# Kernel optimization log

Measured on AMD Instinct MI355X. Metric: run time of the kernel, lower is better.

The kernel has to match this reference:

```python
import jax, jax.numpy as jnp
import numpy as np

N = 50000   # nodes
E = 800000  # edges
IN, HID, OUT, H = 128, 256, 128, 4
C1 = HID // H  # per-head channels for conv1/conv2
EPS_LN = 1e-5


def layer_norm(x, g, b):
    mu = x.mean(-1, keepdims=True)
    var = ((x - mu) ** 2).mean(-1, keepdims=True)
    return (x - mu) * jax.lax.rsqrt(var + EPS_LN) * g + b


def gatv2(x, src, dst, edge_attr, Wl, bl, Wr, br, We, att, bias, heads, ch, n):
    # PyG GATv2Conv (concat=True, negative_slope=0.2, share_weights=False)
    xl = (x @ Wl + bl).reshape(-1, heads, ch)   # [N,H,C] source transform
    xr = (x @ Wr + br).reshape(-1, heads, ch)   # [N,H,C] target transform
    e = (edge_attr @ We).reshape(-1, heads, ch) # [E,H,C] edge transform (no bias)
    m = jax.nn.leaky_relu(xl[src] + xr[dst] + e, 0.2)     # [E,H,C]
    logits = jnp.einsum('ehc,hc->eh', m, att)             # [E,H]
    mx = jax.ops.segment_max(logits, dst, num_segments=n) # segment softmax over dst
    a = jnp.exp(logits - mx[dst])
    denom = jax.ops.segment_sum(a, dst, num_segments=n)
    alpha = a / (denom[dst] + 1e-16)                      # [E,H]
    out = jax.ops.segment_sum(xl[src] * alpha[..., None], dst, num_segments=n)
    return out.reshape(-1, heads * ch) + bias


def setup_inputs() -> dict:
    key = jax.random.key(0)
    ks = jax.random.split(key, 24)
    s = 0.05
    inp = {
        'x': jax.random.normal(ks[0], (N, IN), jnp.float32),
        'edge_index': jax.random.randint(ks[1], (2, E), 0, N, jnp.int32),
        'edge_attr': jax.random.uniform(ks[2], (E, 1), jnp.float32),
        # conv1: in=IN, out per head=C1, heads=H
        'Wl1': jax.random.normal(ks[3], (IN, HID)) * s,  'bl1': jnp.zeros((HID,)),
        'Wr1': jax.random.normal(ks[4], (IN, HID)) * s,  'br1': jnp.zeros((HID,)),
        'We1': jax.random.normal(ks[5], (1, HID)) * s,
        'att1': jax.random.normal(ks[6], (H, C1)) * s,   'bo1': jnp.zeros((HID,)),
        'g1': jnp.ones((HID,)), 'be1': jnp.zeros((HID,)),
        # conv2: in=HID
        'Wl2': jax.random.normal(ks[7], (HID, HID)) * s, 'bl2': jnp.zeros((HID,)),
        'Wr2': jax.random.normal(ks[8], (HID, HID)) * s, 'br2': jnp.zeros((HID,)),
        'We2': jax.random.normal(ks[9], (1, HID)) * s,
        'att2': jax.random.normal(ks[10], (H, C1)) * s,  'bo2': jnp.zeros((HID,)),
        'g2': jnp.ones((HID,)), 'be2': jnp.zeros((HID,)),
        # conv3: heads=1, out=OUT
        'Wl3': jax.random.normal(ks[11], (HID, OUT)) * s, 'bl3': jnp.zeros((OUT,)),
        'Wr3': jax.random.normal(ks[12], (HID, OUT)) * s, 'br3': jnp.zeros((OUT,)),
        'We3': jax.random.normal(ks[13], (1, OUT)) * s,
        'att3': jax.random.normal(ks[14], (1, OUT)) * s,  'bo3': jnp.zeros((OUT,)),
        'g3': jnp.ones((OUT,)), 'be3': jnp.zeros((OUT,)),
    }
    return inp


def reference(x, edge_index, edge_attr,
              Wl1, bl1, Wr1, br1, We1, att1, bo1, g1, be1,
              Wl2, bl2, Wr2, br2, We2, att2, bo2, g2, be2,
              Wl3, bl3, Wr3, br3, We3, att3, bo3, g3, be3):
    src, dst = edge_index[0], edge_index[1]
    h = gatv2(x, src, dst, edge_attr, Wl1, bl1, Wr1, br1, We1, att1, bo1, H, C1, N)
    h = jax.nn.elu(layer_norm(h, g1, be1))  # dropout inactive at inference
    h = gatv2(h, src, dst, edge_attr, Wl2, bl2, Wr2, br2, We2, att2, bo2, H, C1, N)
    h = jax.nn.elu(layer_norm(h, g2, be2))
    h = gatv2(h, src, dst, edge_attr, Wl3, bl3, Wr3, br3, We3, att3, bo3, 1, OUT, N)
    return layer_norm(h, g3, be3)
```

## Files before the change

### kernel.cpp

```cpp
#include <hip/hip_runtime.h>
#include <cstdint>
#include <cstddef>

typedef unsigned short u16;
typedef __attribute__((ext_vector_type(8))) short short8v;
typedef __attribute__((ext_vector_type(4))) float f32x4;

#define IN_DIM 128
#define HID_DIM 256
#define OUT_DIM 128
#define HEADS 4

__device__ __forceinline__ float b2f(u16 v) {
    return __uint_as_float(((unsigned)v) << 16);
}
__device__ __forceinline__ u16 f2b(float f) {
    unsigned u = __float_as_uint(f);
    u += 0x7fffu + ((u >> 16) & 1u);
    return (u16)(u >> 16);
}


__global__ void count_k(const int* __restrict__ dst, int* __restrict__ counts, int ne) {
    int i = blockIdx.x * blockDim.x + threadIdx.x;
    if (i < ne) atomicAdd(&counts[dst[i]], 1);
}

__global__ __launch_bounds__(256) void scanA(const int* __restrict__ counts,
                                             int* __restrict__ bsum, int n) {
    __shared__ int ws[4];
    int blk = blockIdx.x, tid = threadIdx.x;
    int i0 = blk * 1024 + tid * 4;
    int s = 0;
#pragma unroll
    for (int j = 0; j < 4; j++) { int i = i0 + j; if (i < n) s += counts[i]; }
#pragma unroll
    for (int o = 1; o < 64; o <<= 1) s += __shfl_xor(s, o);
    int wv = tid >> 6, ln = tid & 63;
    if (ln == 0) ws[wv] = s;
    __syncthreads();
    if (tid == 0) bsum[blk] = ws[0] + ws[1] + ws[2] + ws[3];
}

__global__ __launch_bounds__(64) void scanB(int* __restrict__ bsum, int nb) {
    int ln = threadIdx.x;
    int carry = 0;
    for (int base = 0; base < nb; base += 64) {
        int i = base + ln;
        int v = (i < nb) ? bsum[i] : 0;
        int x = v;
#pragma unroll
        for (int o = 1; o < 64; o <<= 1) { int t = __shfl_up(x, o); if (ln >= o) x += t; }
        if (i < nb) bsum[i] = carry + x - v;
        carry += __shfl(x, 63);
    }
}

__global__ __launch_bounds__(256) void scanC(const int* __restrict__ counts,
                                             const int* __restrict__ bsum,
                                             int* __restrict__ offs, int* __restrict__ cursor,
                                             int n) {
    __shared__ int wtot[4];
    int blk = blockIdx.x, tid = threadIdx.x, wv = tid >> 6, ln = tid & 63;
    int i0 = blk * 1024 + tid * 4;
    int c[4]; int s = 0;
#pragma unroll
    for (int j = 0; j < 4; j++) { int i = i0 + j; c[j] = (i < n) ? counts[i] : 0; s += c[j]; }
    int x = s;
#pragma unroll
    for (int o = 1; o < 64; o <<= 1) { int t = __shfl_up(x, o); if (ln >= o) x += t; }
    if (ln == 63) wtot[wv] = x;
    int lpref = x - s;
    __syncthreads();
    int wbase = 0;
    for (int i = 0; i < wv; i++) wbase += wtot[i];
    int base = bsum[blk] + wbase + lpref;
#pragma unroll
    for (int j = 0; j < 4; j++) {
        int i = i0 + j;
        if (i < n) {
            offs[i] = base; cursor[i] = base; base += c[j];
            if (i == n - 1) offs[n] = base;
        }
    }
}

__global__ void fill_k(const int* __restrict__ src, const int* __restrict__ dst,
                       const float* __restrict__ ea, int* __restrict__ cursor,
                       int2* __restrict__ cedge, int ne) {
    int i = blockIdx.x * blockDim.x + threadIdx.x;
    if (i < ne) {
        int p = atomicAdd(&cursor[dst[i]], 1);
        int2 t;
        t.x = src[i];
        t.y = __float_as_int(ea[i]);
        cedge[p] = t;
    }
}


template <int KG>
__global__ void xpack_k(const float* __restrict__ X, short* __restrict__ Xp, int total) {
    int gid = blockIdx.x * blockDim.x + threadIdx.x;
    if (gid >= total) return;
    int lane = gid & 63;
    int kg = (gid >> 6) % KG;
    int rt = gid / (64 * KG);
    int row = rt * 16 + (lane & 15);
    int k0 = kg * 32 + ((lane >> 4) << 3);
    const float* src = X + (size_t)row * (KG * 32) + k0;
    short8v o;
#pragma unroll
    for (int j = 0; j < 8; j++) o[j] = (short)f2b(src[j]);
    ((short8v*)Xp)[gid] = o;
}

template <int K, int HOUT>
__global__ void packw_k(const float* __restrict__ Wl, const float* __restrict__ Wr,
                        short* __restrict__ Wp) {
    constexpr int KG = K / 32;
    int gid = blockIdx.x * blockDim.x + threadIdx.x;
    int lane = gid & 63;
    int kg = (gid >> 6) % KG;
    int nt = gid / (64 * KG);
    int col = nt * 16 + (lane & 15);
    int k0 = kg * 32 + ((lane >> 4) << 3);
    const float* Wsrc = (col < HOUT) ? Wl : Wr;
    int c2 = (col < HOUT) ? col : col - HOUT;
    short8v o;
#pragma unroll
    for (int j = 0; j < 8; j++) o[j] = (short)f2b(Wsrc[(size_t)(k0 + j) * HOUT + c2]);
    ((short8v*)Wp)[gid] = o;
}


template <int KG, int NT, int HOUT, int R>
__global__ __launch_bounds__(256) void gemm_mfma(
    const short* __restrict__ Xp, const short* __restrict__ Wp,
    const float* __restrict__ bl, const float* __restrict__ br,
    u16* __restrict__ XL, u16* __restrict__ XR, int nrt) {
    constexpr int NCG = NT / 8;
    int w = threadIdx.x >> 6, lane = threadIdx.x & 63;
    int xcd = blockIdx.x & 7;
    int s = blockIdx.x >> 3;
    int cg = s % NCG;
    int rtg = xcd + 8 * (s / NCG);
    int rt0 = rtg * R;
    if (rt0 >= nrt) return;
    int rcnt = min(R, nrt - rt0);
    int nt0 = cg * 8 + w * 2;
    const short8v* wb = (const short8v*)Wp + lane;
    short8v wf0[KG], wf1[KG];
#pragma unroll
    for (int kg = 0; kg < KG; kg++) {
        wf0[kg] = wb[(size_t)(nt0 * KG + kg) * 64];
        wf1[kg] = wb[(size_t)((nt0 + 1) * KG + kg) * 64];
    }
    int colg0 = nt0 * 16 + ((lane >> 4) << 2);
    int colg1 = colg0 + 16;
    bool isr0 = colg0 >= HOUT;
    bool isr1 = colg1 >= HOUT;
    int cl0 = colg0 - (isr0 ? HOUT : 0);
    int cl1 = colg1 - (isr1 ? HOUT : 0);
    float4 bb0 = *(const float4*)((isr0 ? br : bl) + cl0);
    float4 bb1 = *(const float4*)((isr1 ? br : bl) + cl1);
    u16* ob0 = (isr0 ? XR : XL) + cl0;
    u16* ob1 = (isr1 ? XR : XL) + cl1;

    const short8v* xb = (const short8v*)Xp + (size_t)rt0 * KG * 64 + lane;
    for (int r = 0; r < rcnt; ++r) {
        f32x4 acc0 = {0.f, 0.f, 0.f, 0.f}, acc1 = {0.f, 0.f, 0.f, 0.f};
#pragma unroll
        for (int kg = 0; kg < KG; kg++) {
            short8v xf = xb[(size_t)(r * KG + kg) * 64];
            acc0 = __builtin_amdgcn_mfma_f32_16x16x32_bf16(wf0[kg], xf, acc0, 0, 0, 0);
            acc1 = __builtin_amdgcn_mfma_f32_16x16x32_bf16(wf1[kg], xf, acc1, 0, 0, 0);
        }
        size_t rowoff = (size_t)((rt0 + r) * 16 + (lane & 15)) * HOUT;
        ushort4 o0 = { f2b(acc0[0] + bb0.x), f2b(acc0[1] + bb0.y),
                       f2b(acc0[2] + bb0.z), f2b(acc0[3] + bb0.w) };
        *(ushort4*)(ob0 + rowoff) = o0;
        ushort4 o1 = { f2b(acc1[0] + bb1.x), f2b(acc1[1] + bb1.y),
                       f2b(acc1[2] + bb1.z), f2b(acc1[3] + bb1.w) };
        *(ushort4*)(ob1 + rowoff) = o1;
    }
}


__global__ __launch_bounds__(256) void gat_fused4(
    const int* __restrict__ offs, const int2* __restrict__ cedge,
    const float* __restrict__ We, const float* __restrict__ att,
    const u16* __restrict__ XL, const u16* __restrict__ XR,
    const float* __restrict__ bo, const float* __restrict__ g, const float* __restrict__ be,
    u16* __restrict__ hp, int n) {
    __shared__ int   sS[4][64];
    __shared__ float sEA[4][64];
    int tid = threadIdx.x;
    int w = tid >> 6;
    int lane = tid & 63;
    int node = blockIdx.x * 4 + w;
    int es = lane >> 5;
    int ls = lane & 31;
    int cabs = ls * 8;
    float xr[8], wev[8], atv[8];
    {
        short8v x8 = *(const short8v*)(XR + (size_t)node * 256 + cabs);
        float4 wA = *(const float4*)(We + cabs), wB = *(const float4*)(We + cabs + 4);
        float4 aA = *(const float4*)(att + cabs), aB = *(const float4*)(att + cabs + 4);
#pragma unroll
        for (int i = 0; i < 8; i++) xr[i] = b2f((u16)x8[i]);
        wev[0] = wA.x; wev[1] = wA.y; wev[2] = wA.z; wev[3] = wA.w;
        wev[4] = wB.x; wev[5] = wB.y; wev[6] = wB.z; wev[7] = wB.w;
        atv[0] = aA.x; atv[1] = aA.y; atv[2] = aA.z; atv[3] = aA.w;
        atv[4] = aB.x; atv[5] = aB.y; atv[6] = aB.z; atv[7] = aB.w;
    }
    int b0 = offs[node], eEnd = offs[node + 1];
    float dsum = 0.f;
    float acc[8];
#pragma unroll
    for (int i = 0; i < 8; i++) acc[i] = 0.f;
    for (int base = b0; base < eEnd; base += 64) {
        int cnt = min(64, eEnd - base);
        if (lane < cnt) {
            int2 t = cedge[base + lane];
            sS[w][lane] = t.x;
            sEA[w][lane] = __int_as_float(t.y);
        }
        short8v r0, r1, r2;
        float e0, e1f, e2;
        bool v0, v1, v2;
        {
            int j0 = es, j1 = es + 2, j2 = es + 4;
            v0 = j0 < cnt; v1 = j1 < cnt; v2 = j2 < cnt;
            int i0 = v0 ? j0 : 0, i1 = v1 ? j1 : 0, i2 = v2 ? j2 : 0;
            e0 = sEA[w][i0]; r0 = *(const short8v*)(XL + (size_t)sS[w][i0] * 256 + cabs);
            e1f = sEA[w][i1]; r1 = *(const short8v*)(XL + (size_t)sS[w][i1] * 256 + cabs);
            e2 = sEA[w][i2]; r2 = *(const short8v*)(XL + (size_t)sS[w][i2] * 256 + cabs);
        }
        for (int r = 0; r < cnt; r += 2) {
            short8v rc = r0; float ec = e0; bool vc = v0;
            r0 = r1; e0 = e1f; v0 = v1;
            r1 = r2; e1f = e2; v1 = v2;
            int jn = r + 6 + es;
            v2 = jn < cnt;
            int idx = v2 ? jn : 0;
            e2 = sEA[w][idx];
            r2 = *(const short8v*)(XL + (size_t)sS[w][idx] * 256 + cabs);
            float x[8];
#pragma unroll
            for (int i = 0; i < 8; i++) x[i] = b2f((u16)rc[i]);
            float p = 0.f;
#pragma unroll
            for (int i = 0; i < 8; i++) {
                float t = fmaf(ec, wev[i], x[i]) + xr[i];
                t = fmaxf(t, 0.2f * t);
                p += t * atv[i];
            }
            p += __shfl_xor(p, 1);
            p += __shfl_xor(p, 2);
            p += __shfl_xor(p, 4);
            float wv2 = vc ? __expf(p) : 0.f;
            dsum += wv2;
#pragma unroll
            for (int i = 0; i < 8; i++) acc[i] += wv2 * x[i];
        }
    }
    dsum += __shfl_xor(dsum, 32);
#pragma unroll
    for (int i = 0; i < 8; i++) acc[i] += __shfl_xor(acc[i], 32);
    float inv = 1.f / (dsum + 1e-16f);
    float4 bA = *(const float4*)(bo + cabs), bB = *(const float4*)(bo + cabs + 4);
    float v[8];
    v[0] = acc[0] * inv + bA.x; v[1] = acc[1] * inv + bA.y;
    v[2] = acc[2] * inv + bA.z; v[3] = acc[3] * inv + bA.w;
    v[4] = acc[4] * inv + bB.x; v[5] = acc[5] * inv + bB.y;
    v[6] = acc[6] * inv + bB.z; v[7] = acc[7] * inv + bB.w;
    float s1 = 0.f, s2 = 0.f;
#pragma unroll
    for (int i = 0; i < 8; i++) { s1 += v[i]; s2 += v[i] * v[i]; }
#pragma unroll
    for (int o = 16; o >= 1; o >>= 1) {
        s1 += __shfl_xor(s1, o);
        s2 += __shfl_xor(s2, o);
    }
    float mu = s1 / 256.f;
    float sinv = rsqrtf(s2 / 256.f - mu * mu + 1e-5f);
    if (es == 0) {
        float4 gA = *(const float4*)(g + cabs), gB = *(const float4*)(g + cabs + 4);
        float4 eA = *(const float4*)(be + cabs), eB = *(const float4*)(be + cabs + 4);
        float gg[8] = {gA.x, gA.y, gA.z, gA.w, gB.x, gB.y, gB.z, gB.w};
        float ee[8] = {eA.x, eA.y, eA.z, eA.w, eB.x, eB.y, eB.z, eB.w};
        short8v yv;
#pragma unroll
        for (int i = 0; i < 8; i++) {
            float y = (v[i] - mu) * sinv * gg[i] + ee[i];
            y = (y > 0.f) ? y : expm1f(y);
            yv[i] = (short)f2b(y);
        }
        int kg = cabs >> 5;
        int l = (node & 15) | (((cabs >> 3) & 3) << 4);
        size_t eoff = (((size_t)(node >> 4) * 8 + kg) * 64 + l) * 8;
        *(short8v*)(hp + eoff) = yv;
    }
}


__global__ __launch_bounds__(256) void gat_fused1(
    const int* __restrict__ offs, const int2* __restrict__ cedge,
    const float* __restrict__ We, const float* __restrict__ att,
    const u16* __restrict__ XL, const u16* __restrict__ XR,
    const float* __restrict__ bo, const float* __restrict__ g, const float* __restrict__ be,
    float* __restrict__ out, int n) {
    __shared__ int   sS[4][64];
    __shared__ float sEA[4][64];
    int tid = threadIdx.x;
    int w = tid >> 6;
    int lane = tid & 63;
    int node = blockIdx.x * 4 + w;
    int q = lane >> 4;
    int ls = lane & 15;
    int cb = ls * 8;
    float xr[8], wev[8], atv[8];
    {
        short8v x8 = *(const short8v*)(XR + (size_t)node * 128 + cb);
        float4 wA = *(const float4*)(We + cb), wB = *(const float4*)(We + cb + 4);
        float4 aA = *(const float4*)(att + cb), aB = *(const float4*)(att + cb + 4);
#pragma unroll
        for (int i = 0; i < 8; i++) xr[i] = b2f((u16)x8[i]);
        wev[0] = wA.x; wev[1] = wA.y; wev[2] = wA.z; wev[3] = wA.w;
        wev[4] = wB.x; wev[5] = wB.y; wev[6] = wB.z; wev[7] = wB.w;
        atv[0] = aA.x; atv[1] = aA.y; atv[2] = aA.z; atv[3] = aA.w;
        atv[4] = aB.x; atv[5] = aB.y; atv[6] = aB.z; atv[7] = aB.w;
    }
    int b0 = offs[node], eEnd = offs[node + 1];
    float dsum = 0.f;
    float acc[8];
#pragma unroll
    for (int i = 0; i < 8; i++) acc[i] = 0.f;
    for (int base = b0; base < eEnd; base += 64) {
        int cnt = min(64, eEnd - base);
        if (lane < cnt) {
            int2 t = cedge[base + lane];
            sS[w][lane] = t.x;
            sEA[w][lane] = __int_as_float(t.y);
        }
        short8v r0, r1, r2;
        float e0, e1f, e2;
        bool v0, v1, v2;
        {
            int j0 = q, j1 = q + 4, j2 = q + 8;
            v0 = j0 < cnt; v1 = j1 < cnt; v2 = j2 < cnt;
            int i0 = v0 ? j0 : 0, i1 = v1 ? j1 : 0, i2 = v2 ? j2 : 0;
            e0 = sEA[w][i0]; r0 = *(const short8v*)(XL + (size_t)sS[w][i0] * 128 + cb);
            e1f = sEA[w][i1]; r1 = *(const short8v*)(XL + (size_t)sS[w][i1] * 128 + cb);
            e2 = sEA[w][i2]; r2 = *(const short8v*)(XL + (size_t)sS[w][i2] * 128 + cb);
        }
        for (int r = 0; r < cnt; r += 4) {
            short8v rc = r0; float ec = e0; bool vc = v0;
            r0 = r1; e0 = e1f; v0 = v1;
            r1 = r2; e1f = e2; v1 = v2;
            int jn = r + 12 + q;
            v2 = jn < cnt;
            int idx = v2 ? jn : 0;
            e2 = sEA[w][idx];
            r2 = *(const short8v*)(XL + (size_t)sS[w][idx] * 128 + cb);
            float x[8];
#pragma unroll
            for (int i = 0; i < 8; i++) x[i] = b2f((u16)rc[i]);
            float p = 0.f;
#pragma unroll
            for (int i = 0; i < 8; i++) {
                float t = fmaf(ec, wev[i], x[i]) + xr[i];
                t = fmaxf(t, 0.2f * t);
                p += t * atv[i];
            }
            p += __shfl_xor(p, 1);
            p += __shfl_xor(p, 2);
            p += __shfl_xor(p, 4);
            p += __shfl_xor(p, 8);
            float wv2 = vc ? __expf(p) : 0.f;
            dsum += wv2;
#pragma unroll
            for (int i = 0; i < 8; i++) acc[i] += wv2 * x[i];
        }
    }
    dsum += __shfl_xor(dsum, 32);
    dsum += __shfl_xor(dsum, 16);
#pragma unroll
    for (int i = 0; i < 8; i++) {
        acc[i] += __shfl_xor(acc[i], 32);
        acc[i] += __shfl_xor(acc[i], 16);
    }
    float inv = 1.f / (dsum + 1e-16f);
    float4 bA = *(const float4*)(bo + cb), bB = *(const float4*)(bo + cb + 4);
    float v[8];
    v[0] = acc[0] * inv + bA.x; v[1] = acc[1] * inv + bA.y;
    v[2] = acc[2] * inv + bA.z; v[3] = acc[3] * inv + bA.w;
    v[4] = acc[4] * inv + bB.x; v[5] = acc[5] * inv + bB.y;
    v[6] = acc[6] * inv + bB.z; v[7] = acc[7] * inv + bB.w;
    float s1 = 0.f, s2 = 0.f;
#pragma unroll
    for (int i = 0; i < 8; i++) { s1 += v[i]; s2 += v[i] * v[i]; }
#pragma unroll
    for (int o = 8; o >= 1; o >>= 1) {
        s1 += __shfl_xor(s1, o);
        s2 += __shfl_xor(s2, o);
    }
    float mu = s1 / 128.f;
    float sinv = rsqrtf(s2 / 128.f - mu * mu + 1e-5f);
    if (q == 0) {
        float4 gA = *(const float4*)(g + cb), gB = *(const float4*)(g + cb + 4);
        float4 eA = *(const float4*)(be + cb), eB = *(const float4*)(be + cb + 4);
        float gg[8] = {gA.x, gA.y, gA.z, gA.w, gB.x, gB.y, gB.z, gB.w};
        float ee[8] = {eA.x, eA.y, eA.z, eA.w, eB.x, eB.y, eB.z, eB.w};
        float4 oA, oB;
        oA.x = (v[0] - mu) * sinv * gg[0] + ee[0];
        oA.y = (v[1] - mu) * sinv * gg[1] + ee[1];
        oA.z = (v[2] - mu) * sinv * gg[2] + ee[2];
        oA.w = (v[3] - mu) * sinv * gg[3] + ee[3];
        oB.x = (v[4] - mu) * sinv * gg[4] + ee[4];
        oB.y = (v[5] - mu) * sinv * gg[5] + ee[5];
        oB.z = (v[6] - mu) * sinv * gg[6] + ee[6];
        oB.w = (v[7] - mu) * sinv * gg[7] + ee[7];
        float* op = out + (size_t)node * 128 + cb;
        *(float4*)op = oA;
        *(float4*)(op + 4) = oB;
    }
}


extern "C" void kernel_launch(void* const* d_in, const int* in_sizes, int n_in,
                              void* d_out, int out_size, void* d_ws, size_t ws_size,
                              hipStream_t stream) {
    const float* x  = (const float*)d_in[0];
    const int*   ei = (const int*)d_in[1];
    const float* ea = (const float*)d_in[2];
    const float *Wl1 = (const float*)d_in[3],  *bl1 = (const float*)d_in[4];
    const float *Wr1 = (const float*)d_in[5],  *br1 = (const float*)d_in[6];
    const float *We1 = (const float*)d_in[7],  *att1 = (const float*)d_in[8];
    const float *bo1 = (const float*)d_in[9],  *g1 = (const float*)d_in[10], *be1 = (const float*)d_in[11];
    const float *Wl2 = (const float*)d_in[12], *bl2 = (const float*)d_in[13];
    const float *Wr2 = (const float*)d_in[14], *br2 = (const float*)d_in[15];
    const float *We2 = (const float*)d_in[16], *att2 = (const float*)d_in[17];
    const float *bo2 = (const float*)d_in[18], *g2 = (const float*)d_in[19], *be2 = (const float*)d_in[20];
    const float *Wl3 = (const float*)d_in[21], *bl3 = (const float*)d_in[22];
    const float *Wr3 = (const float*)d_in[23], *br3 = (const float*)d_in[24];
    const float *We3 = (const float*)d_in[25], *att3 = (const float*)d_in[26];
    const float *bo3 = (const float*)d_in[27], *g3 = (const float*)d_in[28], *be3 = (const float*)d_in[29];

    int n = in_sizes[0] / IN_DIM;
    int e = in_sizes[1] / 2;
    const int* srcv = ei;
    const int* dstv = ei + e;
    int nrt = n / 16;

    char* w = (char*)d_ws;
    size_t off = 0;
    auto take = [&](size_t bytes) -> void* {
        void* p = w + off;
        off = (off + bytes + 255) & ~(size_t)255;
        return p;
    };
    int*   counts = (int*)take((size_t)n * 4);
    int*   cursor = (int*)take((size_t)n * 4);
    int*   offs   = (int*)take((size_t)(n + 1) * 4);
    int*   bsum   = (int*)take(256 * 4);
    int2*  cedge  = (int2*)take((size_t)e * 8);
    u16*   XL     = (u16*)take((size_t)n * HID_DIM * 2);
    u16*   XR     = (u16*)take((size_t)n * HID_DIM * 2);
    short* xpack  = (short*)take((size_t)nrt * 4 * 64 * 8 * 2);
    short* hpack  = (short*)take((size_t)nrt * 8 * 64 * 8 * 2);
    short* wp1    = (short*)take((size_t)32 * 4 * 64 * 8 * 2);
    short* wp2    = (short*)take((size_t)32 * 8 * 64 * 8 * 2);
    short* wp3    = (short*)take((size_t)16 * 8 * 64 * 8 * 2);

    const int TPB = 256;
    int eb = (e + TPB - 1) / TPB;
    int nb = (n + 1023) / 1024;

    hipMemsetAsync(counts, 0, (size_t)n * 4, stream);
    count_k<<<eb, TPB, 0, stream>>>(dstv, counts, e);
    scanA<<<nb, TPB, 0, stream>>>(counts, bsum, n);
    scanB<<<1, 64, 0, stream>>>(bsum, nb);
    scanC<<<nb, TPB, 0, stream>>>(counts, bsum, offs, cursor, n);
    fill_k<<<eb, TPB, 0, stream>>>(srcv, dstv, ea, cursor, cedge, e);

    packw_k<IN_DIM,  HID_DIM><<<32 * 4 * 64 / TPB, TPB, 0, stream>>>(Wl1, Wr1, wp1);
    packw_k<HID_DIM, HID_DIM><<<32 * 8 * 64 / TPB, TPB, 0, stream>>>(Wl2, Wr2, wp2);
    packw_k<HID_DIM, OUT_DIM><<<16 * 8 * 64 / TPB, TPB, 0, stream>>>(Wl3, Wr3, wp3);
    int xtot = nrt * 4 * 64;
    xpack_k<4><<<(xtot + TPB - 1) / TPB, TPB, 0, stream>>>(x, xpack, xtot);

    int nrtg8 = (nrt + 7) / 8;
    int grid12 = 8 * ((nrtg8 + 7) / 8) * 4;
    int nrtg4 = (nrt + 3) / 4;
    int grid3 = 8 * ((nrtg4 + 7) / 8) * 2;

    gemm_mfma<4, 32, HID_DIM, 8><<<grid12, TPB, 0, stream>>>(
        xpack, wp1, bl1, br1, XL, XR, nrt);
    gat_fused4<<<n / 4, 256, 0, stream>>>(
        offs, cedge, We1, att1, XL, XR, bo1, g1, be1, (u16*)hpack, n);

    gemm_mfma<8, 32, HID_DIM, 8><<<grid12, TPB, 0, stream>>>(
        hpack, wp2, bl2, br2, XL, XR, nrt);
    gat_fused4<<<n / 4, 256, 0, stream>>>(
        offs, cedge, We2, att2, XL, XR, bo2, g2, be2, (u16*)hpack, n);

    gemm_mfma<8, 16, OUT_DIM, 4><<<grid3, TPB, 0, stream>>>(
        hpack, wp3, bl3, br3, XL, XR, nrt);
    gat_fused1<<<n / 4, 256, 0, stream>>>(
        offs, cedge, We3, att3, XL, XR, bo3, g3, be3, (float*)d_out, n);
}
```

Baseline: 406.3 us.

## Stage GEMM outputs through LDS for coalesced stores; deepen gather prefetch

The MFMA GEMM epilogue now writes bias-added bf16 results into a double-buffered shared tile. The whole block then writes 16-byte contiguous row segments to global memory, instead of scattered 8-byte stores per lane. The edge aggregation kernel's software pipeline for gathering XL rows grows from 3 to 5 in-flight loads per lane to hide more gather latency. The cost is an extra __syncthreads per row tile, LDS traffic, and higher register pressure in the gather kernel.

```diff
diff --git a/kernel.cpp b/kernel.cpp
--- a/kernel.cpp
+++ b/kernel.cpp
@@ -140,7 +140,9 @@
     const float* __restrict__ bl, const float* __restrict__ br,
     u16* __restrict__ XL, u16* __restrict__ XR, int nrt) {
     constexpr int NCG = NT / 8;
+    __shared__ u16 ost[2][16][132];
     int w = threadIdx.x >> 6, lane = threadIdx.x & 63;
+    int tid = threadIdx.x;
     int xcd = blockIdx.x & 7;
     int s = blockIdx.x >> 3;
     int cg = s % NCG;
@@ -156,16 +158,16 @@
         wf0[kg] = wb[(size_t)(nt0 * KG + kg) * 64];
         wf1[kg] = wb[(size_t)((nt0 + 1) * KG + kg) * 64];
     }
-    int colg0 = nt0 * 16 + ((lane >> 4) << 2);
-    int colg1 = colg0 + 16;
-    bool isr0 = colg0 >= HOUT;
-    bool isr1 = colg1 >= HOUT;
-    int cl0 = colg0 - (isr0 ? HOUT : 0);
-    int cl1 = colg1 - (isr1 ? HOUT : 0);
-    float4 bb0 = *(const float4*)((isr0 ? br : bl) + cl0);
-    float4 bb1 = *(const float4*)((isr1 ? br : bl) + cl1);
-    u16* ob0 = (isr0 ? XR : XL) + cl0;
-    u16* ob1 = (isr1 ? XR : XL) + cl1;
+    int strip0 = cg * 128;
+    bool isr = strip0 >= HOUT;
+    int sb = strip0 - (isr ? HOUT : 0);
+    u16* ob = (isr ? XR : XL) + sb;
+    int cl0 = w * 32 + ((lane >> 4) << 2);
+    int cl1 = cl0 + 16;
+    float4 bb0 = *(const float4*)((isr ? br : bl) + sb + cl0);
+    float4 bb1 = *(const float4*)((isr ? br : bl) + sb + cl1);
+    int orow = tid >> 4;
+    int ocol = (tid & 15) * 8;
 
     const short8v* xb = (const short8v*)Xp + (size_t)rt0 * KG * 64 + lane;
     for (int r = 0; r < rcnt; ++r) {
@@ -176,13 +178,20 @@
             acc0 = __builtin_amdgcn_mfma_f32_16x16x32_bf16(wf0[kg], xf, acc0, 0, 0, 0);
             acc1 = __builtin_amdgcn_mfma_f32_16x16x32_bf16(wf1[kg], xf, acc1, 0, 0, 0);
         }
-        size_t rowoff = (size_t)((rt0 + r) * 16 + (lane & 15)) * HOUT;
-        ushort4 o0 = { f2b(acc0[0] + bb0.x), f2b(acc0[1] + bb0.y),
-                       f2b(acc0[2] + bb0.z), f2b(acc0[3] + bb0.w) };
-        *(ushort4*)(ob0 + rowoff) = o0;
-        ushort4 o1 = { f2b(acc1[0] + bb1.x), f2b(acc1[1] + bb1.y),
-                       f2b(acc1[2] + bb1.z), f2b(acc1[3] + bb1.w) };
-        *(ushort4*)(ob1 + rowoff) = o1;
+        int b = r & 1;
+        int row = lane & 15;
+        u16* l0 = &ost[b][row][cl0];
+        l0[0] = f2b(acc0[0] + bb0.x); l0[1] = f2b(acc0[1] + bb0.y);
+        l0[2] = f2b(acc0[2] + bb0.z); l0[3] = f2b(acc0[3] + bb0.w);
+        u16* l1 = &ost[b][row][cl1];
+        l1[0] = f2b(acc1[0] + bb1.x); l1[1] = f2b(acc1[1] + bb1.y);
+        l1[2] = f2b(acc1[2] + bb1.z); l1[3] = f2b(acc1[3] + bb1.w);
+        __syncthreads();
+        ushort4 v0 = *(ushort4*)&ost[b][orow][ocol];
+        ushort4 v1 = *(ushort4*)&ost[b][orow][ocol + 4];
+        u16* gp = ob + (size_t)((rt0 + r) * 16 + orow) * HOUT + ocol;
+        *(ushort4*)gp = v0;
+        *(ushort4*)(gp + 4) = v1;
     }
 }
 
@@ -226,26 +235,31 @@
             sS[w][lane] = t.x;
             sEA[w][lane] = __int_as_float(t.y);
         }
-        short8v r0, r1, r2;
-        float e0, e1f, e2;
-        bool v0, v1, v2;
+        short8v r0, r1, r2, r3, r4;
+        float e0, e1f, e2, e3, e4;
+        bool v0, v1, v2, v3, v4;
         {
-            int j0 = es, j1 = es + 2, j2 = es + 4;
-            v0 = j0 < cnt; v1 = j1 < cnt; v2 = j2 < cnt;
+            int j0 = es, j1 = es + 2, j2 = es + 4, j3 = es + 6, j4 = es + 8;
+            v0 = j0 < cnt; v1 = j1 < cnt; v2 = j2 < cnt; v3 = j3 < cnt; v4 = j4 < cnt;
             int i0 = v0 ? j0 : 0, i1 = v1 ? j1 : 0, i2 = v2 ? j2 : 0;
+            int i3 = v3 ? j3 : 0, i4 = v4 ? j4 : 0;
             e0 = sEA[w][i0]; r0 = *(const short8v*)(XL + (size_t)sS[w][i0] * 256 + cabs);
             e1f = sEA[w][i1]; r1 = *(const short8v*)(XL + (size_t)sS[w][i1] * 256 + cabs);
             e2 = sEA[w][i2]; r2 = *(const short8v*)(XL + (size_t)sS[w][i2] * 256 + cabs);
+            e3 = sEA[w][i3]; r3 = *(const short8v*)(XL + (size_t)sS[w][i3] * 256 + cabs);
+            e4 = sEA[w][i4]; r4 = *(const short8v*)(XL + (size_t)sS[w][i4] * 256 + cabs);
         }
         for (int r = 0; r < cnt; r += 2) {
             short8v rc = r0; float ec = e0; bool vc = v0;
             r0 = r1; e0 = e1f; v0 = v1;
             r1 = r2; e1f = e2; v1 = v2;
-            int jn = r + 6 + es;
-            v2 = jn < cnt;
-            int idx = v2 ? jn : 0;
-            e2 = sEA[w][idx];
-            r2 = *(const short8v*)(XL + (size_t)sS[w][idx] * 256 + cabs);
+            r2 = r3; e2 = e3; v2 = v3;
+            r3 = r4; e3 = e4; v3 = v4;
+            int jn = r + 10 + es;
+            v4 = jn < cnt;
+            int idx = v4 ? jn : 0;
+            e4 = sEA[w][idx];
+            r4 = *(const short8v*)(XL + (size_t)sS[w][idx] * 256 + cabs);
             float x[8];
 #pragma unroll
             for (int i = 0; i < 8; i++) x[i] = b2f((u16)rc[i]);
```

Result: no change. 410.0 us (+0.9%).
